# Kernel optimization log

Measured on AMD Instinct MI355X. Metric: run time of the kernel, lower is better.

## Reference

```python
import jax, jax.numpy as jnp
import numpy as np

N, D, D_QK, D_V = 8192, 1024, 128, 128

def setup_inputs() -> dict:
    key = jax.random.key(0)
    k1, k2, k3, k4 = jax.random.split(key, 4)
    s = 1.0 / np.sqrt(D)
    return {
        "x": jax.random.normal(k1, (N, D), dtype=jnp.float32),
        "Wq": jax.random.normal(k2, (D_QK, D), dtype=jnp.float32) * s,
        "Wk": jax.random.normal(k3, (D_QK, D), dtype=jnp.float32) * s,
        "Wv": jax.random.normal(k4, (D_V, D), dtype=jnp.float32) * s,
    }

def reference(x, Wq, Wk, Wv):
    # NOTE: original code MULTIPLIES by sqrt(D_qk) (dq_sqrt_inv = np.sqrt(D_qk)).
    scale = jnp.sqrt(jnp.asarray(D_QK, dtype=x.dtype))
    q = x @ Wq.T            # [N, D_qk]
    k = x @ Wk.T            # [N, D_qk]
    v = x @ Wv.T            # [N, D_v]
    scores = scale * (q @ k.T)          # [N, N]
    attn = jax.nn.softmax(scores, axis=-1)
    return attn @ v          # [N, D_v]
```

## Files before the change

kernel.cpp:

```cpp
#include <hip/hip_runtime.h>
#include <hip/hip_bf16.h>
#include <math.h>
#include <stdint.h>

#define N_TOK 8192
#define D_IN  1024
#define D_H   128
#define SPLIT 8

typedef __bf16 bf16;
typedef __attribute__((ext_vector_type(4))) __bf16 bf16x4;
typedef __attribute__((ext_vector_type(8))) __bf16 bf16x8;
typedef __attribute__((ext_vector_type(4))) float floatx4;

#define MFMA16(a, b, c) __builtin_amdgcn_mfma_f32_16x16x32_bf16((a), (b), (c), 0, 0, 0)

#define QSCALE 16.322625246404958f

__device__ __forceinline__ uint32_t pack2(float a, float b) {
    union { bf16 h[2]; uint32_t u; } z;
    z.h[0] = (bf16)a; z.h[1] = (bf16)b; return z.u;
}

__device__ __forceinline__ size_t vtf_idx(int n, int d) {
    return ((size_t)((n >> 6) * 8 + (d >> 4)) << 10)
         + (((n >> 3) & 7) << 7) + ((d & 15) << 3) + (n & 7);
}
__device__ __forceinline__ size_t khf_idx(int n, int d) {
    return ((size_t)(((n >> 6) * 4 + (d >> 5)) * 4 + ((n >> 4) & 3)) << 9)
         + (((d >> 3) & 3) << 7) + ((n & 15) << 3) + (d & 7);
}

#define X_OCT (N_TOK * D_IN / 8)
#define W_OCT (3 * D_H * D_IN / 8)

__global__ __launch_bounds__(256)
void convert_kernel(const float* __restrict__ x,
                    const float* __restrict__ Wq,
                    const float* __restrict__ Wk,
                    const float* __restrict__ Wv,
                    bf16* __restrict__ xhf, bf16* __restrict__ xlf,
                    bf16* __restrict__ whf, bf16* __restrict__ wlf)
{
    const int gid = blockIdx.x * 256 + threadIdx.x;
    const float* src;
    bf16 *dh, *dl;
    size_t doff;
    if (gid < X_OCT) {
        int lane = gid & 63, fc = gid >> 6;
        int kc = fc & 31, mt = fc >> 5;
        int n  = mt * 16 + (lane & 15);
        int k0 = kc * 32 + ((lane >> 4) << 3);
        src = x + (size_t)n * D_IN + k0;
        dh = xhf; dl = xlf; doff = (size_t)gid << 3;
    } else {
        int w = gid - X_OCT;
        int y = w >> 14, r = w & 16383;
        int lane = r & 63, fc = r >> 6;
        int kc = fc & 31, ct = fc >> 5;
        int col = ct * 16 + (lane & 15);
        int k0  = kc * 32 + ((lane >> 4) << 3);
        const float* W = (y == 0) ? Wq : (y == 1) ? Wk : Wv;
        src = W + (size_t)col * D_IN + k0;
        dh = whf; dl = wlf; doff = (size_t)w << 3;
    }
    float4 a = *(const float4*)src;
    float4 b = *(const float4*)(src + 4);
    float vv[8] = { a.x, a.y, a.z, a.w, b.x, b.y, b.z, b.w };
    bf16x8 h, l;
    #pragma unroll
    for (int j = 0; j < 8; ++j) {
        bf16 hh = (bf16)vv[j];
        h[j] = hh;
        l[j] = (bf16)(vv[j] - (float)hh);
    }
    *(bf16x8*)(dh + doff) = h;
    *(bf16x8*)(dl + doff) = l;
}

__global__ __launch_bounds__(256)
void qkv_kernel(const bf16* __restrict__ xhf, const bf16* __restrict__ xlf,
                const bf16* __restrict__ whf, const bf16* __restrict__ wlf,
                bf16* __restrict__ q_hi, bf16* __restrict__ q_lo,
                bf16* __restrict__ khf, bf16* __restrict__ klf,
                bf16* __restrict__ vtf)
{
    __shared__ bf16 w_s[2][16384];

    const int t    = threadIdx.x;
    const int lane = t & 63;
    const int wid  = t >> 6;
    const int wr   = wid >> 1;
    const int wc   = wid & 1;
    const int lid  = lane & 15;
    const int quad = lane >> 4;
    const int m0   = blockIdx.x * 64;
    const bf16* wh = whf + ((size_t)blockIdx.y << 17);
    const bf16* wl = wlf + ((size_t)blockIdx.y << 17);

    auto stage = [&](int c0, int buf) {
        #pragma unroll
        for (int i = 0; i < 8; ++i) {
            int p   = wid * 8 + i;
            int hl  = p >> 4, ct = (p >> 1) & 7, kci = p & 1;
            const bf16* src = (hl ? wl : wh)
                            + ((size_t)(ct * 32 + c0 + kci) << 9) + (lane << 3);
            bf16* dst = &w_s[buf][p << 9];
            __builtin_amdgcn_global_load_lds(
                (const __attribute__((address_space(1))) void*)src,
                (__attribute__((address_space(3))) void*)dst, 16, 0, 0);
        }
    };

    floatx4 acc[2][4];
    #pragma unroll
    for (int m = 0; m < 2; ++m)
        #pragma unroll
        for (int ct = 0; ct < 4; ++ct)
            #pragma unroll
            for (int r = 0; r < 4; ++r) acc[m][ct][r] = 0.f;

    stage(0, 0);

    for (int c = 0; c < 16; ++c) {
        const int c0 = c * 2;
        const int cb = c & 1;
        __syncthreads();
        if (c < 15) stage(c0 + 2, cb ^ 1);

        #pragma unroll
        for (int kci = 0; kci < 2; ++kci) {
            bf16x8 ah[2], al[2];
            #pragma unroll
            for (int m = 0; m < 2; ++m) {
                int mt = (m0 >> 4) + wr * 2 + m;
                const size_t xb = ((size_t)(mt * 32 + c0 + kci) << 9) + (lane << 3);
                ah[m] = *(const bf16x8*)(xhf + xb);
                al[m] = *(const bf16x8*)(xlf + xb);
            }
            #pragma unroll
            for (int ct = 0; ct < 4; ++ct) {
                const int pb = (((wc * 4 + ct) * 2 + kci) << 9) + (lane << 3);
                bf16x8 bh = *(const bf16x8*)&w_s[cb][pb];
                bf16x8 bl = *(const bf16x8*)&w_s[cb][(16 << 9) + pb];
                #pragma unroll
                for (int m = 0; m < 2; ++m) {
                    acc[m][ct] = MFMA16(ah[m], bh, acc[m][ct]);
                    acc[m][ct] = MFMA16(al[m], bh, acc[m][ct]);
                    acc[m][ct] = MFMA16(ah[m], bl, acc[m][ct]);
                }
            }
        }
    }

    if (blockIdx.y == 0) {
        #pragma unroll
        for (int s2 = 0; s2 < 2; ++s2)
            #pragma unroll
            for (int ct = 0; ct < 4; ++ct)
                #pragma unroll
                for (int r = 0; r < 4; ++r) {
                    int row = m0 + wr * 32 + s2 * 16 + quad * 4 + r;
                    int col = wc * 64 + ct * 16 + lid;
                    float a = acc[s2][ct][r] * QSCALE;
                    bf16 h = (bf16)a;
                    q_hi[(size_t)row * D_H + col] = h;
                    q_lo[(size_t)row * D_H + col] = (bf16)(a - (float)h);
                }
    } else if (blockIdx.y == 1) {
        #pragma unroll
        for (int s2 = 0; s2 < 2; ++s2)
            #pragma unroll
            for (int ct = 0; ct < 4; ++ct)
                #pragma unroll
                for (int r = 0; r < 4; ++r) {
                    int n = m0 + wr * 32 + s2 * 16 + quad * 4 + r;
                    int d = wc * 64 + ct * 16 + lid;
                    float a = acc[s2][ct][r];
                    bf16 h = (bf16)a;
                    size_t idx = khf_idx(n, d);
                    khf[idx] = h;
                    klf[idx] = (bf16)(a - (float)h);
                }
    } else {
        #pragma unroll
        for (int s2 = 0; s2 < 2; ++s2)
            #pragma unroll
            for (int ct = 0; ct < 4; ++ct)
                #pragma unroll
                for (int r = 0; r < 4; ++r) {
                    int n = m0 + wr * 32 + s2 * 16 + quad * 4 + r;
                    int d = wc * 64 + ct * 16 + lid;
                    vtf[vtf_idx(n, d)] = (bf16)acc[s2][ct][r];
                }
    }
}

#define BQ   128
#define BKEY 64

__global__ __launch_bounds__(256, 2)
void flash_kernel(const bf16* __restrict__ qh, const bf16* __restrict__ ql,
                  const bf16* __restrict__ khf, const bf16* __restrict__ klf,
                  const bf16* __restrict__ vtf,
                  bf16*  __restrict__ opart,
                  float* __restrict__ mpart,
                  float* __restrict__ lpart)
{
    __shared__ bf16 k_s[2][16384];

    const int t     = threadIdx.x;
    const int lane  = t & 63;
    const int wid   = t >> 6;
    const int lid   = lane & 15;
    const int quad  = lane >> 4;
    const int q0    = blockIdx.x * BQ;
    const int strip = wid * 32;
    const int sp    = blockIdx.y;
    const int tile0 = sp * (N_TOK / BKEY / SPLIT);
    const int tile1 = tile0 + (N_TOK / BKEY / SPLIT);

    bf16x8 b_hi[2][4], b_lo[2][4];
    #pragma unroll
    for (int ct = 0; ct < 2; ++ct) {
        const size_t rowb = (size_t)(q0 + strip + ct * 16 + lid) * D_H + quad * 8;
        #pragma unroll
        for (int kc = 0; kc < 4; ++kc) {
            b_hi[ct][kc] = *(const bf16x8*)(qh + rowb + kc * 32);
            b_lo[ct][kc] = *(const bf16x8*)(ql + rowb + kc * 32);
        }
    }

    bf16x8 vones;
    #pragma unroll
    for (int j = 0; j < 8; ++j) vones[j] = (bf16)1.0f;

    float m_run[2] = { -INFINITY, -INFINITY };
    floatx4 l_acc[2];
    #pragma unroll
    for (int ct = 0; ct < 2; ++ct)
        #pragma unroll
        for (int r = 0; r < 4; ++r) l_acc[ct][r] = 0.f;
    floatx4 o_acc[8][2];
    #pragma unroll
    for (int dt = 0; dt < 8; ++dt)
        #pragma unroll
        for (int ct = 0; ct < 2; ++ct)
            #pragma unroll
            for (int r = 0; r < 4; ++r) o_acc[dt][ct][r] = 0.f;

    auto stage = [&](int tile, int buf) {
        const bf16* gh = khf + ((size_t)tile << 13) + (wid << 11) + (lane << 3);
        const bf16* gl = klf + ((size_t)tile << 13) + (wid << 11) + (lane << 3);
        bf16* lh = &k_s[buf][wid << 11];
        bf16* ll = lh + 8192;
        #pragma unroll
        for (int i = 0; i < 4; ++i) {
            __builtin_amdgcn_global_load_lds(
                (const __attribute__((address_space(1))) void*)(gh + i * 512),
                (__attribute__((address_space(3))) void*)(lh + i * 512), 16, 0, 0);
            __builtin_amdgcn_global_load_lds(
                (const __attribute__((address_space(1))) void*)(gl + i * 512),
                (__attribute__((address_space(3))) void*)(ll + i * 512), 16, 0, 0);
        }
    };

    stage(tile0, 0);

    for (int tt = tile0; tt < tile1; ++tt) {
        const int cb = (tt - tile0) & 1;
        __syncthreads();
        if (tt + 1 < tile1) stage(tt + 1, cb ^ 1);

        const bf16* khp = &k_s[cb][0];
        const bf16* klp = &k_s[cb][8192];
        floatx4 s[4][2];
        #pragma unroll
        for (int mt = 0; mt < 4; ++mt)
            #pragma unroll
            for (int ct = 0; ct < 2; ++ct)
                #pragma unroll
                for (int r = 0; r < 4; ++r) s[mt][ct][r] = 0.f;

        #pragma unroll
        for (int kc = 0; kc < 4; ++kc)
            #pragma unroll
            for (int mt = 0; mt < 4; ++mt) {
                const int fo = ((kc * 4 + mt) << 9) + (lane << 3);
                bf16x8 ah = *(const bf16x8*)&khp[fo];
                bf16x8 al = *(const bf16x8*)&klp[fo];
                #pragma unroll
                for (int ct = 0; ct < 2; ++ct) {
                    s[mt][ct] = MFMA16(ah, b_hi[ct][kc], s[mt][ct]);
                    s[mt][ct] = MFMA16(al, b_hi[ct][kc], s[mt][ct]);
                    s[mt][ct] = MFMA16(ah, b_lo[ct][kc], s[mt][ct]);
                }
            }

        const bf16* vb = vtf + ((size_t)tt << 13) + (lane << 3);
        bf16x8 vf0[8];
        #pragma unroll
        for (int dt = 0; dt < 8; ++dt)
            vf0[dt] = *(const bf16x8*)(vb + ((size_t)dt << 10));

        float alpha[2];
        uint32_t u0[4][2], u1[4][2];
        #pragma unroll
        for (int ct = 0; ct < 2; ++ct) {
            float mx = s[0][ct][0];
            #pragma unroll
            for (int mt = 0; mt < 4; ++mt)
                #pragma unroll
                for (int r = 0; r < 4; ++r)
                    mx = fmaxf(mx, s[mt][ct][r]);
            mx = fmaxf(mx, __shfl_xor(mx, 16, 64));
            mx = fmaxf(mx, __shfl_xor(mx, 32, 64));
            float mn = fmaxf(m_run[ct], mx);
            alpha[ct] = exp2f(m_run[ct] - mn);
            m_run[ct] = mn;
            #pragma unroll
            for (int mt = 0; mt < 4; ++mt) {
                float p0 = exp2f(s[mt][ct][0] - mn);
                float p1 = exp2f(s[mt][ct][1] - mn);
                float p2 = exp2f(s[mt][ct][2] - mn);
                float p3 = exp2f(s[mt][ct][3] - mn);
                u0[mt][ct] = pack2(p0, p1);
                u1[mt][ct] = pack2(p2, p3);
            }
        }

        bf16x8 pB[2][2];
        {
            const int lsrc = ((quad & 1) << 5) + lid;
            const bool himt = (quad & 2) != 0;
            #pragma unroll
            for (int kc2 = 0; kc2 < 2; ++kc2)
                #pragma unroll
                for (int ct = 0; ct < 2; ++ct) {
                    const int mA = kc2 * 2, mB = kc2 * 2 + 1;
                    uint32_t w0a = __shfl((int)u0[mA][ct], lsrc, 64);
                    uint32_t w0b = __shfl((int)u0[mB][ct], lsrc, 64);
                    uint32_t w1a = __shfl((int)u1[mA][ct], lsrc, 64);
                    uint32_t w1b = __shfl((int)u1[mB][ct], lsrc, 64);
                    uint32_t w2a = __shfl((int)u0[mA][ct], lsrc + 16, 64);
                    uint32_t w2b = __shfl((int)u0[mB][ct], lsrc + 16, 64);
                    uint32_t w3a = __shfl((int)u1[mA][ct], lsrc + 16, 64);
                    uint32_t w3b = __shfl((int)u1[mB][ct], lsrc + 16, 64);
                    union { uint32_t w[4]; bf16x8 v; } z;
                    z.w[0] = himt ? w0b : w0a;
                    z.w[1] = himt ? w1b : w1a;
                    z.w[2] = himt ? w2b : w2a;
                    z.w[3] = himt ? w3b : w3a;
                    pB[kc2][ct] = z.v;
                }
        }

        bf16x8 vf1[8];
        #pragma unroll
        for (int dt = 0; dt < 8; ++dt)
            vf1[dt] = *(const bf16x8*)(vb + ((size_t)dt << 10) + 512);

        if (__any(alpha[0] != 1.0f || alpha[1] != 1.0f)) {
            #pragma unroll
            for (int ct = 0; ct < 2; ++ct) {
                #pragma unroll
                for (int r = 0; r < 4; ++r) l_acc[ct][r] *= alpha[ct];
                #pragma unroll
                for (int dt = 0; dt < 8; ++dt)
                    #pragma unroll
                    for (int r = 0; r < 4; ++r)
                        o_acc[dt][ct][r] *= alpha[ct];
            }
        }

        #pragma unroll
        for (int ct = 0; ct < 2; ++ct) {
            l_acc[ct] = MFMA16(vones, pB[0][ct], l_acc[ct]);
            l_acc[ct] = MFMA16(vones, pB[1][ct], l_acc[ct]);
        }
        #pragma unroll
        for (int dt = 0; dt < 8; ++dt)
            #pragma unroll
            for (int ct = 0; ct < 2; ++ct) {
                o_acc[dt][ct] = MFMA16(vf0[dt], pB[0][ct], o_acc[dt][ct]);
                o_acc[dt][ct] = MFMA16(vf1[dt], pB[1][ct], o_acc[dt][ct]);
            }
    }

    uint32_t* opw = (uint32_t*)(opart + (size_t)sp * N_TOK * D_H);
    #pragma unroll
    for (int dt = 0; dt < 8; ++dt)
        #pragma unroll
        for (int ct = 0; ct < 2; ++ct) {
            int qrow  = q0 + strip + ct * 16 + lid;
            int dbase = dt * 16 + quad * 4;
            opw[(qrow * D_H + dbase) >> 1]     = pack2(o_acc[dt][ct][0], o_acc[dt][ct][1]);
            opw[(qrow * D_H + dbase + 2) >> 1] = pack2(o_acc[dt][ct][2], o_acc[dt][ct][3]);
        }
    if (quad == 0) {
        #pragma unroll
        for (int ct = 0; ct < 2; ++ct) {
            int row = q0 + strip + ct * 16 + lid;
            mpart[(size_t)sp * N_TOK + row] = m_run[ct];
            lpart[(size_t)sp * N_TOK + row] = l_acc[ct][0];
        }
    }
}

__global__ __launch_bounds__(256)
void combine_kernel(const bf16* __restrict__ opart,
                    const float* __restrict__ mpart,
                    const float* __restrict__ lpart,
                    float* __restrict__ out)
{
    const int t   = threadIdx.x;
    const int row = blockIdx.x * 16 + (t >> 4);
    const int c0  = (t & 15) * 8;

    float ms[SPLIT], ls[SPLIT];
    float mstar = -INFINITY;
    #pragma unroll
    for (int s = 0; s < SPLIT; ++s) {
        ms[s] = mpart[(size_t)s * N_TOK + row];
        ls[s] = lpart[(size_t)s * N_TOK + row];
        mstar = fmaxf(mstar, ms[s]);
    }
    float acc[8] = {};
    float L = 0.f;
    #pragma unroll
    for (int s = 0; s < SPLIT; ++s) {
        float w = exp2f(ms[s] - mstar);
        L += w * ls[s];
        bf16x8 o = *(const bf16x8*)&opart[((size_t)s * N_TOK + row) * D_H + c0];
        #pragma unroll
        for (int j = 0; j < 8; ++j)
            acc[j] += w * (float)o[j];
    }
    float inv = 1.f / L;
    float* dst = &out[(size_t)row * D_H + c0];
    *(float4*)(dst + 0) = make_float4(acc[0] * inv, acc[1] * inv,
                                      acc[2] * inv, acc[3] * inv);
    *(float4*)(dst + 4) = make_float4(acc[4] * inv, acc[5] * inv,
                                      acc[6] * inv, acc[7] * inv);
}

extern "C" void kernel_launch(void* const* d_in, const int* in_sizes, int n_in,
                              void* d_out, int out_size, void* d_ws, size_t ws_size,
                              hipStream_t stream) {
    const float* x  = (const float*)d_in[0];
    const float* Wq = (const float*)d_in[1];
    const float* Wk = (const float*)d_in[2];
    const float* Wv = (const float*)d_in[3];
    float* out = (float*)d_out;

    bf16* wsb = (bf16*)d_ws;
    const size_t SZ = (size_t)N_TOK * D_H;
    bf16* xhf = wsb;
    bf16* xlf = xhf + (size_t)X_OCT * 8;
    bf16* whf = xlf + (size_t)X_OCT * 8;
    bf16* wlf = whf + (size_t)W_OCT * 8;
    bf16* qh  = wlf + (size_t)W_OCT * 8;
    bf16* ql  = qh + SZ;
    bf16* khf = ql + SZ;
    bf16* klf = khf + SZ;
    bf16* vtf = klf + SZ;
    bf16* opart = vtf + SZ;
    float* mpart = (float*)(opart + (size_t)SPLIT * SZ);
    float* lpart = mpart + (size_t)SPLIT * N_TOK;

    convert_kernel<<<dim3((X_OCT + W_OCT) / 256), 256, 0, stream>>>(
        x, Wq, Wk, Wv, xhf, xlf, whf, wlf);
    qkv_kernel<<<dim3(N_TOK / 64, 3), 256, 0, stream>>>(
        xhf, xlf, whf, wlf, qh, ql, khf, klf, vtf);
    flash_kernel<<<dim3(N_TOK / BQ, SPLIT), 256, 0, stream>>>(
        qh, ql, khf, klf, vtf, opart, mpart, lpart);
    combine_kernel<<<dim3(N_TOK / 16), 256, 0, stream>>>(opart, mpart, lpart, out);
}
```

Measured before the change: 191.2 us.

## Drop LDS staging in QKV and flash kernels, load operands directly from global

```diff
diff --git a/kernel.cpp b/kernel.cpp
--- a/kernel.cpp
+++ b/kernel.cpp
@@ -78,121 +78,69 @@
     *(bf16x8*)(dl + doff) = l;
 }
 
-__global__ __launch_bounds__(256)
+__global__ __launch_bounds__(512)
 void qkv_kernel(const bf16* __restrict__ xhf, const bf16* __restrict__ xlf,
                 const bf16* __restrict__ whf, const bf16* __restrict__ wlf,
                 bf16* __restrict__ q_hi, bf16* __restrict__ q_lo,
                 bf16* __restrict__ khf, bf16* __restrict__ klf,
                 bf16* __restrict__ vtf)
 {
-    __shared__ bf16 w_s[2][16384];
-
     const int t    = threadIdx.x;
     const int lane = t & 63;
     const int wid  = t >> 6;
-    const int wr   = wid >> 1;
-    const int wc   = wid & 1;
     const int lid  = lane & 15;
     const int quad = lane >> 4;
-    const int m0   = blockIdx.x * 64;
-    const bf16* wh = whf + ((size_t)blockIdx.y << 17);
-    const bf16* wl = wlf + ((size_t)blockIdx.y << 17);
-
-    auto stage = [&](int c0, int buf) {
-        #pragma unroll
-        for (int i = 0; i < 8; ++i) {
-            int p   = wid * 8 + i;
-            int hl  = p >> 4, ct = (p >> 1) & 7, kci = p & 1;
-            const bf16* src = (hl ? wl : wh)
-                            + ((size_t)(ct * 32 + c0 + kci) << 9) + (lane << 3);
-            bf16* dst = &w_s[buf][p << 9];
-            __builtin_amdgcn_global_load_lds(
-                (const __attribute__((address_space(1))) void*)src,
-                (__attribute__((address_space(3))) void*)dst, 16, 0, 0);
-        }
-    };
-
-    floatx4 acc[2][4];
-    #pragma unroll
-    for (int m = 0; m < 2; ++m)
-        #pragma unroll
-        for (int ct = 0; ct < 4; ++ct)
-            #pragma unroll
-            for (int r = 0; r < 4; ++r) acc[m][ct][r] = 0.f;
-
-    stage(0, 0);
-
-    for (int c = 0; c < 16; ++c) {
-        const int c0 = c * 2;
-        const int cb = c & 1;
-        __syncthreads();
-        if (c < 15) stage(c0 + 2, cb ^ 1);
-
-        #pragma unroll
-        for (int kci = 0; kci < 2; ++kci) {
-            bf16x8 ah[2], al[2];
-            #pragma unroll
-            for (int m = 0; m < 2; ++m) {
-                int mt = (m0 >> 4) + wr * 2 + m;
-                const size_t xb = ((size_t)(mt * 32 + c0 + kci) << 9) + (lane << 3);
-                ah[m] = *(const bf16x8*)(xhf + xb);
-                al[m] = *(const bf16x8*)(xlf + xb);
+    const int mt   = blockIdx.x * 2 + (wid & 1);
+    const int ctg0 = (wid >> 1) * 6;
+
+    floatx4 acc[6];
+    #pragma unroll
+    for (int j = 0; j < 6; ++j)
+        #pragma unroll
+        for (int r = 0; r < 4; ++r) acc[j][r] = 0.f;
+
+    #pragma unroll 4
+    for (int kc = 0; kc < 32; ++kc) {
+        const size_t xb = ((size_t)(mt * 32 + kc) << 9) + (lane << 3);
+        bf16x8 ah = *(const bf16x8*)(xhf + xb);
+        bf16x8 al = *(const bf16x8*)(xlf + xb);
+        #pragma unroll
+        for (int j = 0; j < 6; ++j) {
+            const int ctg = ctg0 + j;
+            const int y = ctg >> 3, ct = ctg & 7;
+            const size_t wb = ((size_t)y << 17)
+                            + ((size_t)(ct * 32 + kc) << 9) + (lane << 3);
+            bf16x8 bh = *(const bf16x8*)(whf + wb);
+            bf16x8 bl = *(const bf16x8*)(wlf + wb);
+            acc[j] = MFMA16(ah, bh, acc[j]);
+            acc[j] = MFMA16(al, bh, acc[j]);
+            acc[j] = MFMA16(ah, bl, acc[j]);
+        }
+    }
+
+    #pragma unroll
+    for (int j = 0; j < 6; ++j) {
+        const int ctg = ctg0 + j;
+        const int y = ctg >> 3, ct = ctg & 7;
+        #pragma unroll
+        for (int r = 0; r < 4; ++r) {
+            const int row = mt * 16 + quad * 4 + r;
+            const int col = ct * 16 + lid;
+            float a = acc[j][r];
+            if (y == 0) {
+                a *= QSCALE;
+                bf16 h = (bf16)a;
+                q_hi[(size_t)row * D_H + col] = h;
+                q_lo[(size_t)row * D_H + col] = (bf16)(a - (float)h);
+            } else if (y == 1) {
+                bf16 h = (bf16)a;
+                size_t idx = khf_idx(row, col);
+                khf[idx] = h;
+                klf[idx] = (bf16)(a - (float)h);
+            } else {
+                vtf[vtf_idx(row, col)] = (bf16)a;
             }
-            #pragma unroll
-            for (int ct = 0; ct < 4; ++ct) {
-                const int pb = (((wc * 4 + ct) * 2 + kci) << 9) + (lane << 3);
-                bf16x8 bh = *(const bf16x8*)&w_s[cb][pb];
-                bf16x8 bl = *(const bf16x8*)&w_s[cb][(16 << 9) + pb];
-                #pragma unroll
-                for (int m = 0; m < 2; ++m) {
-                    acc[m][ct] = MFMA16(ah[m], bh, acc[m][ct]);
-                    acc[m][ct] = MFMA16(al[m], bh, acc[m][ct]);
-                    acc[m][ct] = MFMA16(ah[m], bl, acc[m][ct]);
-                }
-            }
-        }
-    }
-
-    if (blockIdx.y == 0) {
-        #pragma unroll
-        for (int s2 = 0; s2 < 2; ++s2)
-            #pragma unroll
-            for (int ct = 0; ct < 4; ++ct)
-                #pragma unroll
-                for (int r = 0; r < 4; ++r) {
-                    int row = m0 + wr * 32 + s2 * 16 + quad * 4 + r;
-                    int col = wc * 64 + ct * 16 + lid;
-                    float a = acc[s2][ct][r] * QSCALE;
-                    bf16 h = (bf16)a;
-                    q_hi[(size_t)row * D_H + col] = h;
-                    q_lo[(size_t)row * D_H + col] = (bf16)(a - (float)h);
-                }
-    } else if (blockIdx.y == 1) {
-        #pragma unroll
-        for (int s2 = 0; s2 < 2; ++s2)
-            #pragma unroll
-            for (int ct = 0; ct < 4; ++ct)
-                #pragma unroll
-                for (int r = 0; r < 4; ++r) {
-                    int n = m0 + wr * 32 + s2 * 16 + quad * 4 + r;
-                    int d = wc * 64 + ct * 16 + lid;
-                    float a = acc[s2][ct][r];
-                    bf16 h = (bf16)a;
-                    size_t idx = khf_idx(n, d);
-                    khf[idx] = h;
-                    klf[idx] = (bf16)(a - (float)h);
-                }
-    } else {
-        #pragma unroll
-        for (int s2 = 0; s2 < 2; ++s2)
-            #pragma unroll
-            for (int ct = 0; ct < 4; ++ct)
-                #pragma unroll
-                for (int r = 0; r < 4; ++r) {
-                    int n = m0 + wr * 32 + s2 * 16 + quad * 4 + r;
-                    int d = wc * 64 + ct * 16 + lid;
-                    vtf[vtf_idx(n, d)] = (bf16)acc[s2][ct][r];
-                }
+        }
     }
 }
 
@@ -207,16 +155,14 @@
                   float* __restrict__ mpart,
                   float* __restrict__ lpart)
 {
-    __shared__ bf16 k_s[2][16384];
-
     const int t     = threadIdx.x;
     const int lane  = t & 63;
     const int wid   = t >> 6;
     const int lid   = lane & 15;
     const int quad  = lane >> 4;
-    const int q0    = blockIdx.x * BQ;
+    const int sp    = blockIdx.x & 7;
+    const int q0    = (blockIdx.x >> 3) * BQ;
     const int strip = wid * 32;
-    const int sp    = blockIdx.y;
     const int tile0 = sp * (N_TOK / BKEY / SPLIT);
     const int tile1 = tile0 + (N_TOK / BKEY / SPLIT);
 
@@ -249,31 +195,10 @@
             #pragma unroll
             for (int r = 0; r < 4; ++r) o_acc[dt][ct][r] = 0.f;
 
-    auto stage = [&](int tile, int buf) {
-        const bf16* gh = khf + ((size_t)tile << 13) + (wid << 11) + (lane << 3);
-        const bf16* gl = klf + ((size_t)tile << 13) + (wid << 11) + (lane << 3);
-        bf16* lh = &k_s[buf][wid << 11];
-        bf16* ll = lh + 8192;
-        #pragma unroll
-        for (int i = 0; i < 4; ++i) {
-            __builtin_amdgcn_global_load_lds(
-                (const __attribute__((address_space(1))) void*)(gh + i * 512),
-                (__attribute__((address_space(3))) void*)(lh + i * 512), 16, 0, 0);
-            __builtin_amdgcn_global_load_lds(
-                (const __attribute__((address_space(1))) void*)(gl + i * 512),
-                (__attribute__((address_space(3))) void*)(ll + i * 512), 16, 0, 0);
-        }
-    };
-
-    stage(tile0, 0);
-
     for (int tt = tile0; tt < tile1; ++tt) {
-        const int cb = (tt - tile0) & 1;
-        __syncthreads();
-        if (tt + 1 < tile1) stage(tt + 1, cb ^ 1);
-
-        const bf16* khp = &k_s[cb][0];
-        const bf16* klp = &k_s[cb][8192];
+        const bf16* kbh = khf + ((size_t)tt << 13);
+        const bf16* kbl = klf + ((size_t)tt << 13);
+
         floatx4 s[4][2];
         #pragma unroll
         for (int mt = 0; mt < 4; ++mt)
@@ -283,25 +208,23 @@
                 for (int r = 0; r < 4; ++r) s[mt][ct][r] = 0.f;
 
         #pragma unroll
-        for (int kc = 0; kc < 4; ++kc)
+        for (int kc = 0; kc < 4; ++kc) {
+            bf16x8 ah[4], al[4];
             #pragma unroll
             for (int mt = 0; mt < 4; ++mt) {
                 const int fo = ((kc * 4 + mt) << 9) + (lane << 3);
-                bf16x8 ah = *(const bf16x8*)&khp[fo];
-                bf16x8 al = *(const bf16x8*)&klp[fo];
+                ah[mt] = *(const bf16x8*)(kbh + fo);
+                al[mt] = *(const bf16x8*)(kbl + fo);
+            }
+            #pragma unroll
+            for (int mt = 0; mt < 4; ++mt)
                 #pragma unroll
                 for (int ct = 0; ct < 2; ++ct) {
-                    s[mt][ct] = MFMA16(ah, b_hi[ct][kc], s[mt][ct]);
-                    s[mt][ct] = MFMA16(al, b_hi[ct][kc], s[mt][ct]);
-                    s[mt][ct] = MFMA16(ah, b_lo[ct][kc], s[mt][ct]);
+                    s[mt][ct] = MFMA16(ah[mt], b_hi[ct][kc], s[mt][ct]);
+                    s[mt][ct] = MFMA16(al[mt], b_hi[ct][kc], s[mt][ct]);
+                    s[mt][ct] = MFMA16(ah[mt], b_lo[ct][kc], s[mt][ct]);
                 }
-            }
-
-        const bf16* vb = vtf + ((size_t)tt << 13) + (lane << 3);
-        bf16x8 vf0[8];
-        #pragma unroll
-        for (int dt = 0; dt < 8; ++dt)
-            vf0[dt] = *(const bf16x8*)(vb + ((size_t)dt << 10));
+        }
 
         float alpha[2];
         uint32_t u0[4][2], u1[4][2];
@@ -355,10 +278,11 @@
                 }
         }
 
-        bf16x8 vf1[8];
+        const bf16* vb = vtf + ((size_t)tt << 13) + (lane << 3);
+        bf16x8 vf0[8];
         #pragma unroll
         for (int dt = 0; dt < 8; ++dt)
-            vf1[dt] = *(const bf16x8*)(vb + ((size_t)dt << 10) + 512);
+            vf0[dt] = *(const bf16x8*)(vb + ((size_t)dt << 10));
 
         if (__any(alpha[0] != 1.0f || alpha[1] != 1.0f)) {
             #pragma unroll
@@ -374,17 +298,26 @@
         }
 
         #pragma unroll
-        for (int ct = 0; ct < 2; ++ct) {
+        for (int ct = 0; ct < 2; ++ct)
             l_acc[ct] = MFMA16(vones, pB[0][ct], l_acc[ct]);
+        #pragma unroll
+        for (int dt = 0; dt < 8; ++dt)
+            #pragma unroll
+            for (int ct = 0; ct < 2; ++ct)
+                o_acc[dt][ct] = MFMA16(vf0[dt], pB[0][ct], o_acc[dt][ct]);
+
+        bf16x8 vf1[8];
+        #pragma unroll
+        for (int dt = 0; dt < 8; ++dt)
+            vf1[dt] = *(const bf16x8*)(vb + ((size_t)dt << 10) + 512);
+        #pragma unroll
+        for (int ct = 0; ct < 2; ++ct)
             l_acc[ct] = MFMA16(vones, pB[1][ct], l_acc[ct]);
-        }
         #pragma unroll
         for (int dt = 0; dt < 8; ++dt)
             #pragma unroll
-            for (int ct = 0; ct < 2; ++ct) {
-                o_acc[dt][ct] = MFMA16(vf0[dt], pB[0][ct], o_acc[dt][ct]);
+            for (int ct = 0; ct < 2; ++ct)
                 o_acc[dt][ct] = MFMA16(vf1[dt], pB[1][ct], o_acc[dt][ct]);
-            }
     }
 
     uint32_t* opw = (uint32_t*)(opart + (size_t)sp * N_TOK * D_H);
@@ -470,9 +403,9 @@
 
     convert_kernel<<<dim3((X_OCT + W_OCT) / 256), 256, 0, stream>>>(
         x, Wq, Wk, Wv, xhf, xlf, whf, wlf);
-    qkv_kernel<<<dim3(N_TOK / 64, 3), 256, 0, stream>>>(
+    qkv_kernel<<<dim3(N_TOK / 32), 512, 0, stream>>>(
         xhf, xlf, whf, wlf, qh, ql, khf, klf, vtf);
-    flash_kernel<<<dim3(N_TOK / BQ, SPLIT), 256, 0, stream>>>(
+    flash_kernel<<<dim3((N_TOK / BQ) * SPLIT), 256, 0, stream>>>(
         qh, ql, khf, klf, vtf, opart, mpart, lpart);
     combine_kernel<<<dim3(N_TOK / 16), 256, 0, stream>>>(opart, mpart, lpart, out);
 }
```

Result: slower. 239.3 us (+25.2%).
